# Kernel optimization log

Hardware: AMD Instinct MI355X
Metric: run time of the kernel (lower is better)

Reference implementation:

```python
import jax, jax.numpy as jnp
import numpy as np

VOCAB, EMB, HID, T = 33, 16, 128, 14

def setup_inputs() -> dict:
    key = jax.random.key(0)
    ks = jax.random.split(key, 12)
    B = 131072
    x = jax.random.randint(ks[0], (B, T), 0, VOCAB, dtype=jnp.int32)
    s = 1.0 / np.sqrt(HID)
    emb_table = jax.random.normal(ks[1], (VOCAB, EMB), dtype=jnp.float32)
    # torch LSTM params: gate order [i, f, g, o], uniform(-1/sqrt(H), 1/sqrt(H))
    W_ih = jax.random.uniform(ks[2], (4 * HID, EMB), minval=-s, maxval=s, dtype=jnp.float32)
    W_hh = jax.random.uniform(ks[3], (4 * HID, HID), minval=-s, maxval=s, dtype=jnp.float32)
    b_ih = jax.random.uniform(ks[4], (4 * HID,), minval=-s, maxval=s, dtype=jnp.float32)
    b_hh = jax.random.uniform(ks[5], (4 * HID,), minval=-s, maxval=s, dtype=jnp.float32)
    W1 = jax.random.uniform(ks[6], (64, 128), minval=-s, maxval=s, dtype=jnp.float32)
    b1 = jax.random.uniform(ks[7], (64,), minval=-s, maxval=s, dtype=jnp.float32)
    W2 = jax.random.uniform(ks[8], (32, 64), minval=-0.125, maxval=0.125, dtype=jnp.float32)
    b2 = jax.random.uniform(ks[9], (32,), minval=-0.125, maxval=0.125, dtype=jnp.float32)
    W3 = jax.random.uniform(ks[10], (2, 32), minval=-0.176, maxval=0.176, dtype=jnp.float32)
    b3 = jax.random.uniform(ks[11], (2,), minval=-0.176, maxval=0.176, dtype=jnp.float32)
    return {"x": x, "emb_table": emb_table, "W_ih": W_ih, "W_hh": W_hh,
            "b_ih": b_ih, "b_hh": b_hh, "W1": W1, "b1": b1,
            "W2": W2, "b2": b2, "W3": W3, "b3": b3}

def reference(x, emb_table, W_ih, W_hh, b_ih, b_hh, W1, b1, W2, b2, W3, b3):
    B = x.shape[0]
    # padding_idx=0: row 0 is zero
    table = emb_table.at[0].set(0.0)
    emb = table[x]                                # [B, T, E]
    # precompute input projections for all timesteps in one GEMM
    x_proj = jnp.einsum('bte,ge->btg', emb, W_ih) + b_ih + b_hh  # [B, T, 4H]

    def step(carry, xp_t):
        h, c = carry
        gates = xp_t + h @ W_hh.T                 # [B, 4H]
        i, f, g, o = jnp.split(gates, 4, axis=-1)
        i, f, o = jax.nn.sigmoid(i), jax.nn.sigmoid(f), jax.nn.sigmoid(o)
        g = jnp.tanh(g)
        c = f * c + i * g
        h = o * jnp.tanh(c)
        return (h, c), None

    h0 = jnp.zeros((B, HID), dtype=emb.dtype)
    c0 = jnp.zeros((B, HID), dtype=emb.dtype)
    (h_last, _), _ = jax.lax.scan(step, (h0, c0), jnp.swapaxes(x_proj, 0, 1))

    y = jax.nn.sigmoid(h_last @ W1.T + b1)
    y = jax.nn.sigmoid(y @ W2.T + b2)
    return y @ W3.T + b3                          # [B, 2]
```

## Files before the change

### kernel.cpp

```cpp
#include <hip/hip_runtime.h>
#include <hip/hip_bf16.h>

#define TSTEP 14
#define BROWS 64
#define KCOMB 160
#define ESTR  16
#define L2E   1.4426950408889634f
#define L2E2  2.8853900817779268f

typedef __attribute__((ext_vector_type(8))) short bf16x8;
typedef __attribute__((ext_vector_type(4))) float f32x4;
typedef __attribute__((ext_vector_type(4))) int   i32x4;

#define MFMA(a,b,c) __builtin_amdgcn_mfma_f32_16x16x32_bf16((a),(b),(c),0,0,0)

__device__ inline ushort f2b(float f){
  union { float f; unsigned u; } v; v.f = f;
  unsigned r = v.u + 0x7fff + ((v.u >> 16) & 1);
  return (ushort)(r >> 16);
}
__device__ inline float rcpf(float x){ return __builtin_amdgcn_rcpf(x); }

#if __has_builtin(__builtin_amdgcn_exp2f)
__device__ inline float EXP2(float x){ return __builtin_amdgcn_exp2f(x); }
#else
__device__ inline float EXP2(float x){ return __expf(x * 0.6931471805599453f); }
#endif

__device__ inline unsigned cvt_pk_bf16(float lo, float hi){
  unsigned r;
  asm("v_cvt_pk_bf16_f32 %0, %1, %2" : "=v"(r) : "v"(lo), "v"(hi));
  return r;
}

__global__ void prep_kernel(const float* __restrict__ W_ih, const float* __restrict__ W_hh,
                            const float* __restrict__ W1,   const float* __restrict__ W2,
                            ushort* __restrict__ wcomb, ushort* __restrict__ w1b, ushort* __restrict__ w2b){
  int i = blockIdx.x * blockDim.x + threadIdx.x;
  if (i < 512*KCOMB){
    int n = i / KCOMB, k = i - n*KCOMB;
    float s = ((n >> 7) == 2) ? L2E2 : L2E;
    float v = (k < 128) ? W_hh[n*128 + k]*s : ((k < 144) ? W_ih[n*16 + (k-128)]*s : 0.f);
    wcomb[i] = f2b(v);
  } else if (i < 512*KCOMB + 64*128){
    int j = i - 512*KCOMB;
    w1b[j] = f2b(W1[j] * L2E);
  } else if (i < 512*KCOMB + 64*128 + 32*64){
    int j = i - 512*KCOMB - 64*128;
    w2b[j] = f2b(W2[j] * L2E);
  }
}

__global__ __attribute__((amdgpu_flat_work_group_size(512, 512), amdgpu_waves_per_eu(2, 2)))
void lstm_kernel(const int* __restrict__ x, const float* __restrict__ emb_table,
                 const float* __restrict__ b_ih, const float* __restrict__ b_hh,
                 const float* __restrict__ b1, const float* __restrict__ b2,
                 const float* __restrict__ W3, const float* __restrict__ b3,
                 const ushort* __restrict__ wcomb, const ushort* __restrict__ w1b,
                 const ushort* __restrict__ w2b, float* __restrict__ out)
{
  __shared__ ushort A_h[2*BROWS*128];
  __shared__ __align__(16) char Ebuf[TSTEP*BROWS*ESTR*2];

  ushort* E  = (ushort*)Ebuf;
  ushort* y1 = (ushort*)Ebuf;
  float*  y2 = (float*)(Ebuf + 8192);

  const int tid  = threadIdx.x;
  const int lane = tid & 63;
  const int w    = tid >> 6;
  const int l15  = lane & 15;
  const int lg   = lane >> 4;
  const int r0   = blockIdx.x * BROWS;

  { i32x4* az = (i32x4*)A_h;
    #pragma unroll
    for (int i = 0; i < 2; ++i) az[tid + i*512] = (i32x4){0,0,0,0}; }

  for (int idx = tid; idx < BROWS*TSTEP; idx += 512){
    int r = idx / TSTEP, t = idx - r*TSTEP;
    int tok = x[(r0 + r)*TSTEP + t];
    int xr  = (r >> 2) & 1;
    unsigned* dst = (unsigned*)(E + (t*BROWS + r)*ESTR);
    if (tok == 0){
      #pragma unroll
      for (int e = 0; e < 8; ++e) dst[e] = 0u;
    } else {
      const float* src = emb_table + tok*16;
      #pragma unroll
      for (int e = 0; e < 8; ++e)
        dst[((e >> 2) ^ xr)*4 + (e & 3)] = cvt_pk_bf16(src[2*e], src[2*e+1]);
    }
  }

  bf16x8 bB[4][5];
  #pragma unroll
  for (int g = 0; g < 4; ++g){
    const int n = g*128 + w*16 + l15;
    #pragma unroll
    for (int kt = 0; kt < 5; ++kt)
      bB[g][kt] = *(const bf16x8*)((const short*)wcomb + n*KCOMB + kt*32 + lg*8);
  }

  f32x4 biasv[4];
  #pragma unroll
  for (int g = 0; g < 4; ++g){
    const int n = g*128 + w*16 + l15;
    float bv = (b_ih[n] + b_hh[n]) * ((g == 2) ? L2E2 : L2E);
    biasv[g] = (f32x4){bv,bv,bv,bv};
  }

  f32x4 cst[4];
  #pragma unroll
  for (int m = 0; m < 4; ++m) cst[m] = (f32x4){0.f,0.f,0.f,0.f};

  const int j2 = w*16 + l15;

  __syncthreads();

  for (int t = 0; t < TSTEP; ++t){
    const ushort* Ar = A_h + (t & 1)*BROWS*128;
    ushort*       Aw = A_h + ((t & 1)^1)*BROWS*128;

    #pragma unroll
    for (int m = 0; m < 4; ++m){
      const int row = m*16 + l15;
      const int swz = (row & 7) << 3;
      const short* base_e = (const short*)Ar + row*128 + ((lg*8) ^ swz);
      const short* base_o = (const short*)Ar + row*128 + ((32 + lg*8) ^ swz);
      bf16x8 aF[5];
      aF[0] = *(const bf16x8*)(base_e);
      aF[1] = *(const bf16x8*)(base_o);
      aF[2] = *(const bf16x8*)(base_e + 64);
      aF[3] = *(const bf16x8*)(base_o + 64);
      aF[4] = *(const bf16x8*)((const short*)E + (t*BROWS + row)*ESTR
                               + (((lg & 1) ^ ((row >> 2) & 1))*8));

      f32x4 acc[4];
      #pragma unroll
      for (int g = 0; g < 4; ++g){
        acc[g] = MFMA(aF[0], bB[g][0], biasv[g]);
        #pragma unroll
        for (int kt = 1; kt < 5; ++kt)
          acc[g] = MFMA(aF[kt], bB[g][kt], acc[g]);
      }

      #pragma unroll
      for (int rp = 0; rp < 2; ++rp){
        float h2[2];
        #pragma unroll
        for (int q = 0; q < 2; ++q){
          const int r = rp*2 + q;
          float iv = rcpf(1.f + EXP2(-acc[0][r]));
          float fv = rcpf(1.f + EXP2(-acc[1][r]));
          float gv = __builtin_fmaf(-2.f, rcpf(EXP2(acc[2][r]) + 1.f), 1.f);
          float ov = rcpf(1.f + EXP2(-acc[3][r]));
          float cv = __builtin_fmaf(fv, cst[m][r], iv*gv);
          cst[m][r] = cv;
          h2[q] = ov * __builtin_fmaf(-2.f, rcpf(EXP2(cv*L2E2) + 1.f), 1.f);
        }
        unsigned u = cvt_pk_bf16(h2[0], h2[1]);
        const int row0 = m*16 + lg*4 + rp*2;
        const int row1 = row0 + 1;
        Aw[row0*128 + (j2 ^ ((row0 & 7) << 3))] = (ushort)u;
        Aw[row1*128 + (j2 ^ ((row1 & 7) << 3))] = (ushort)(u >> 16);
      }
    }

    __syncthreads();
  }

  const ushort* Hf = A_h;

  {
    const int mt = w & 3, nh = w >> 2;
    f32x4 acc1[2];
    #pragma unroll
    for (int nt = 0; nt < 2; ++nt){
      float bv = b1[nh*32 + nt*16 + l15] * L2E;
      acc1[nt] = (f32x4){bv,bv,bv,bv};
    }
    const int arow = mt*16 + l15;
    const int aswz = (arow & 7) << 3;
    const short* abase = (const short*)Hf + arow*128;
    #pragma unroll
    for (int kt = 0; kt < 4; ++kt){
      bf16x8 aF = *(const bf16x8*)(abase + ((kt*32 + lg*8) ^ aswz));
      #pragma unroll
      for (int nt = 0; nt < 2; ++nt){
        const int n = nh*32 + nt*16 + l15;
        bf16x8 bF = *(const bf16x8*)((const short*)w1b + n*128 + kt*32 + lg*8);
        acc1[nt] = MFMA(aF, bF, acc1[nt]);
      }
    }
    #pragma unroll
    for (int nt = 0; nt < 2; ++nt)
      #pragma unroll
      for (int r = 0; r < 4; ++r){
        const int row = mt*16 + lg*4 + r;
        const int col = nh*32 + nt*16 + l15;
        y1[row*64 + (col ^ ((row & 7) << 3))] = f2b(rcpf(1.f + EXP2(-acc1[nt][r])));
      }
  }
  __syncthreads();

  if (w < 4){
    f32x4 acc2[2];
    #pragma unroll
    for (int nt = 0; nt < 2; ++nt){
      float bv = b2[nt*16 + l15] * L2E;
      acc2[nt] = (f32x4){bv,bv,bv,bv};
    }
    const int arow = w*16 + l15;
    const int aswz = (arow & 7) << 3;
    const short* abase = (const short*)y1 + arow*64;
    #pragma unroll
    for (int kt = 0; kt < 2; ++kt){
      bf16x8 aF = *(const bf16x8*)(abase + ((kt*32 + lg*8) ^ aswz));
      #pragma unroll
      for (int nt = 0; nt < 2; ++nt){
        const int n = nt*16 + l15;
        bf16x8 bF = *(const bf16x8*)((const short*)w2b + n*64 + kt*32 + lg*8);
        acc2[nt] = MFMA(aF, bF, acc2[nt]);
      }
    }
    #pragma unroll
    for (int nt = 0; nt < 2; ++nt)
      #pragma unroll
      for (int r = 0; r < 4; ++r){
        const int row = w*16 + lg*4 + r;
        const int col = nt*16 + l15;
        y2[row*33 + col] = rcpf(1.f + EXP2(-acc2[nt][r]));
      }
  }
  __syncthreads();

  if (tid < 128){
    const int lr = tid >> 1, oc = tid & 1;
    float s = b3[oc];
    #pragma unroll
    for (int k = 0; k < 32; ++k)
      s += y2[lr*33 + k] * W3[oc*32 + k];
    out[(size_t)(r0 + lr)*2 + oc] = s;
  }
}

extern "C" void kernel_launch(void* const* d_in, const int* in_sizes, int n_in,
                              void* d_out, int out_size, void* d_ws, size_t ws_size,
                              hipStream_t stream){
  const int*   x    = (const int*)  d_in[0];
  const float* emb  = (const float*)d_in[1];
  const float* W_ih = (const float*)d_in[2];
  const float* W_hh = (const float*)d_in[3];
  const float* b_ih = (const float*)d_in[4];
  const float* b_hh = (const float*)d_in[5];
  const float* W1   = (const float*)d_in[6];
  const float* b1   = (const float*)d_in[7];
  const float* W2   = (const float*)d_in[8];
  const float* b2   = (const float*)d_in[9];
  const float* W3   = (const float*)d_in[10];
  const float* b3   = (const float*)d_in[11];
  float* out = (float*)d_out;

  const int B = in_sizes[0] / TSTEP;

  ushort* wcomb = (ushort*)d_ws;
  ushort* w1b   = wcomb + 512*KCOMB;
  ushort* w2b   = w1b + 64*128;

  const int prep_total = 512*KCOMB + 64*128 + 32*64;
  prep_kernel<<<(prep_total + 255)/256, 256, 0, stream>>>(W_ih, W_hh, W1, W2, wcomb, w1b, w2b);
  lstm_kernel<<<B/BROWS, 512, 0, stream>>>(x, emb, b_ih, b_hh, b1, b2, W3, b3,
                                           wcomb, w1b, w2b, out);
}
```

Before: 377.2 us.

## Process two independent 64-row batch tiles per block to interleave recurrences

Each block now handles 128 batch rows as two independent 64-row tiles, each with its own double-buffered hidden-state LDS region and cell state, interleaved inside the timestep loop. The aim is to let the MFMA work of one tile overlap the transcendental gate math of the other, and to amortise the per-timestep barrier and the register-resident weight loads over twice the rows. The cost is more registers for cell state, double the LDS footprint, and half as many blocks, which may lower occupancy or cause spilling.

```diff
diff --git a/kernel.cpp b/kernel.cpp
--- a/kernel.cpp
+++ b/kernel.cpp
@@ -2,7 +2,7 @@
 #include <hip/hip_bf16.h>
 
 #define TSTEP 14
-#define BROWS 64
+#define BROWS 128
 #define KCOMB 160
 #define ESTR  16
 #define L2E   1.4426950408889634f
@@ -59,12 +59,12 @@
                  const ushort* __restrict__ wcomb, const ushort* __restrict__ w1b,
                  const ushort* __restrict__ w2b, float* __restrict__ out)
 {
-  __shared__ ushort A_h[2*BROWS*128];
-  __shared__ __align__(16) char Ebuf[TSTEP*BROWS*ESTR*2];
+  __shared__ ushort A_h[2*2*64*128];
+  __shared__ __align__(16) char Ebuf[2*TSTEP*64*ESTR*2];
 
   ushort* E  = (ushort*)Ebuf;
   ushort* y1 = (ushort*)Ebuf;
-  float*  y2 = (float*)(Ebuf + 8192);
+  float*  y2 = (float*)(Ebuf + 16384);
 
   const int tid  = threadIdx.x;
   const int lane = tid & 63;
@@ -75,13 +75,17 @@
 
   { i32x4* az = (i32x4*)A_h;
     #pragma unroll
-    for (int i = 0; i < 2; ++i) az[tid + i*512] = (i32x4){0,0,0,0}; }
+    for (int i = 0; i < 2; ++i){
+      az[tid + i*512]        = (i32x4){0,0,0,0};
+      az[2048 + tid + i*512] = (i32x4){0,0,0,0};
+    } }
 
   for (int idx = tid; idx < BROWS*TSTEP; idx += 512){
     int r = idx / TSTEP, t = idx - r*TSTEP;
     int tok = x[(r0 + r)*TSTEP + t];
-    int xr  = (r >> 2) & 1;
-    unsigned* dst = (unsigned*)(E + (t*BROWS + r)*ESTR);
+    int tt = r >> 6, rr = r & 63;
+    int xr  = (rr >> 2) & 1;
+    unsigned* dst = (unsigned*)(E + tt*(TSTEP*64*ESTR) + (t*64 + rr)*ESTR);
     if (tok == 0){
       #pragma unroll
       for (int e = 0; e < 8; ++e) dst[e] = 0u;
@@ -110,101 +114,108 @@
     biasv[g] = (f32x4){bv,bv,bv,bv};
   }
 
-  f32x4 cst[4];
+  f32x4 cst[2][4];
   #pragma unroll
-  for (int m = 0; m < 4; ++m) cst[m] = (f32x4){0.f,0.f,0.f,0.f};
+  for (int tt = 0; tt < 2; ++tt)
+    #pragma unroll
+    for (int m = 0; m < 4; ++m) cst[tt][m] = (f32x4){0.f,0.f,0.f,0.f};
 
   const int j2 = w*16 + l15;
 
   __syncthreads();
 
   for (int t = 0; t < TSTEP; ++t){
-    const ushort* Ar = A_h + (t & 1)*BROWS*128;
-    ushort*       Aw = A_h + ((t & 1)^1)*BROWS*128;
+    const int bufR = t & 1, bufW = bufR ^ 1;
 
     #pragma unroll
     for (int m = 0; m < 4; ++m){
-      const int row = m*16 + l15;
-      const int swz = (row & 7) << 3;
-      const short* base_e = (const short*)Ar + row*128 + ((lg*8) ^ swz);
-      const short* base_o = (const short*)Ar + row*128 + ((32 + lg*8) ^ swz);
-      bf16x8 aF[5];
-      aF[0] = *(const bf16x8*)(base_e);
-      aF[1] = *(const bf16x8*)(base_o);
-      aF[2] = *(const bf16x8*)(base_e + 64);
-      aF[3] = *(const bf16x8*)(base_o + 64);
-      aF[4] = *(const bf16x8*)((const short*)E + (t*BROWS + row)*ESTR
-                               + (((lg & 1) ^ ((row >> 2) & 1))*8));
-
-      f32x4 acc[4];
-      #pragma unroll
-      for (int g = 0; g < 4; ++g){
-        acc[g] = MFMA(aF[0], bB[g][0], biasv[g]);
+      #pragma unroll
+      for (int tt = 0; tt < 2; ++tt){
+        const ushort* Ar = A_h + (tt*2 + bufR)*8192;
+        ushort*       Aw = A_h + (tt*2 + bufW)*8192;
+        const short*  Et = (const short*)E + tt*(TSTEP*64*ESTR) + t*64*ESTR;
+
+        const int row = m*16 + l15;
+        const int swz = (row & 7) << 3;
+        const short* base_e = (const short*)Ar + row*128 + ((lg*8) ^ swz);
+        const short* base_o = (const short*)Ar + row*128 + ((32 + lg*8) ^ swz);
+        bf16x8 aF[5];
+        aF[0] = *(const bf16x8*)(base_e);
+        aF[1] = *(const bf16x8*)(base_o);
+        aF[2] = *(const bf16x8*)(base_e + 64);
+        aF[3] = *(const bf16x8*)(base_o + 64);
+        aF[4] = *(const bf16x8*)(Et + row*ESTR + (((lg & 1) ^ ((row >> 2) & 1))*8));
+
+        f32x4 acc[4];
         #pragma unroll
-        for (int kt = 1; kt < 5; ++kt)
-          acc[g] = MFMA(aF[kt], bB[g][kt], acc[g]);
-      }
-
-      #pragma unroll
-      for (int rp = 0; rp < 2; ++rp){
-        float h2[2];
+        for (int g = 0; g < 4; ++g){
+          acc[g] = MFMA(aF[0], bB[g][0], biasv[g]);
+          #pragma unroll
+          for (int kt = 1; kt < 5; ++kt)
+            acc[g] = MFMA(aF[kt], bB[g][kt], acc[g]);
+        }
+
         #pragma unroll
-        for (int q = 0; q < 2; ++q){
-          const int r = rp*2 + q;
-          float iv = rcpf(1.f + EXP2(-acc[0][r]));
-          float fv = rcpf(1.f + EXP2(-acc[1][r]));
-          float gv = __builtin_fmaf(-2.f, rcpf(EXP2(acc[2][r]) + 1.f), 1.f);
-          float ov = rcpf(1.f + EXP2(-acc[3][r]));
-          float cv = __builtin_fmaf(fv, cst[m][r], iv*gv);
-          cst[m][r] = cv;
-          h2[q] = ov * __builtin_fmaf(-2.f, rcpf(EXP2(cv*L2E2) + 1.f), 1.f);
+        for (int rp = 0; rp < 2; ++rp){
+          float h2[2];
+          #pragma unroll
+          for (int q = 0; q < 2; ++q){
+            const int r = rp*2 + q;
+            float iv = rcpf(1.f + EXP2(-acc[0][r]));
+            float fv = rcpf(1.f + EXP2(-acc[1][r]));
+            float gv = __builtin_fmaf(-2.f, rcpf(EXP2(acc[2][r]) + 1.f), 1.f);
+            float ov = rcpf(1.f + EXP2(-acc[3][r]));
+            float cv = __builtin_fmaf(fv, cst[tt][m][r], iv*gv);
+            cst[tt][m][r] = cv;
+            h2[q] = ov * __builtin_fmaf(-2.f, rcpf(EXP2(cv*L2E2) + 1.f), 1.f);
+          }
+          unsigned u = cvt_pk_bf16(h2[0], h2[1]);
+          const int row0 = m*16 + lg*4 + rp*2;
+          const int row1 = row0 + 1;
+          Aw[row0*128 + (j2 ^ ((row0 & 7) << 3))] = (ushort)u;
+          Aw[row1*128 + (j2 ^ ((row1 & 7) << 3))] = (ushort)(u >> 16);
         }
-        unsigned u = cvt_pk_bf16(h2[0], h2[1]);
-        const int row0 = m*16 + lg*4 + rp*2;
-        const int row1 = row0 + 1;
-        Aw[row0*128 + (j2 ^ ((row0 & 7) << 3))] = (ushort)u;
-        Aw[row1*128 + (j2 ^ ((row1 & 7) << 3))] = (ushort)(u >> 16);
       }
     }
 
     __syncthreads();
   }
 
-  const ushort* Hf = A_h;
 
   {
-    const int mt = w & 3, nh = w >> 2;
-    f32x4 acc1[2];
-    #pragma unroll
-    for (int nt = 0; nt < 2; ++nt){
-      float bv = b1[nh*32 + nt*16 + l15] * L2E;
+    f32x4 acc1[4];
+    #pragma unroll
+    for (int nt = 0; nt < 4; ++nt){
+      float bv = b1[nt*16 + l15] * L2E;
       acc1[nt] = (f32x4){bv,bv,bv,bv};
     }
-    const int arow = mt*16 + l15;
+    const int arowg = w*16 + l15;
+    const ushort* Hf = A_h + ((w >> 2)*2 + 0)*8192;
+    const int arow = arowg & 63;
     const int aswz = (arow & 7) << 3;
     const short* abase = (const short*)Hf + arow*128;
     #pragma unroll
     for (int kt = 0; kt < 4; ++kt){
       bf16x8 aF = *(const bf16x8*)(abase + ((kt*32 + lg*8) ^ aswz));
       #pragma unroll
-      for (int nt = 0; nt < 2; ++nt){
-        const int n = nh*32 + nt*16 + l15;
+      for (int nt = 0; nt < 4; ++nt){
+        const int n = nt*16 + l15;
         bf16x8 bF = *(const bf16x8*)((const short*)w1b + n*128 + kt*32 + lg*8);
         acc1[nt] = MFMA(aF, bF, acc1[nt]);
       }
     }
     #pragma unroll
-    for (int nt = 0; nt < 2; ++nt)
+    for (int nt = 0; nt < 4; ++nt)
       #pragma unroll
       for (int r = 0; r < 4; ++r){
-        const int row = mt*16 + lg*4 + r;
-        const int col = nh*32 + nt*16 + l15;
+        const int row = w*16 + lg*4 + r;
+        const int col = nt*16 + l15;
         y1[row*64 + (col ^ ((row & 7) << 3))] = f2b(rcpf(1.f + EXP2(-acc1[nt][r])));
       }
   }
   __syncthreads();
 
-  if (w < 4){
+  {
     f32x4 acc2[2];
     #pragma unroll
     for (int nt = 0; nt < 2; ++nt){
@@ -235,7 +246,7 @@
   }
   __syncthreads();
 
-  if (tid < 128){
+  if (tid < 256){
     const int lr = tid >> 1, oc = tid & 1;
     float s = b3[oc];
     #pragma unroll
```

Measured after the change: 363.7 us. 3.6% less time.
